# Performance work log

Hardware: AMD Instinct MI355X
Metric: run time of the kernel (lower is better)

## Reference

```python
import jax, jax.numpy as jnp
import numpy as np

B, L, D = 16, 2048, 320          # batch, frames, stacked feature dim (80 mel * 4 reduction)
CODEBOOK_SIZE, CODEBOOK_DIM = 8192, 16


def setup_inputs() -> dict:
    key = jax.random.key(0)
    k1, k2, k3 = jax.random.split(key, 3)
    masked_target_values = jax.random.normal(k1, (B, L, D), dtype=jnp.float32)
    # xavier_uniform_ for shape (D, codebook_dim): bound = sqrt(6/(fan_in+fan_out))
    bound = np.sqrt(6.0 / (D + CODEBOOK_DIM)).astype(np.float32)
    project_mat = jax.random.uniform(k2, (D, CODEBOOK_DIM), dtype=jnp.float32,
                                     minval=-bound, maxval=bound)
    cb = jax.random.normal(k3, (CODEBOOK_SIZE, CODEBOOK_DIM), dtype=jnp.float32)
    codebook_norm = cb / jnp.maximum(jnp.linalg.norm(cb, axis=-1, keepdims=True), 1e-12)
    return {"masked_target_values": masked_target_values,
            "project_mat": project_mat,
            "codebook_norm": codebook_norm}


def reference(masked_target_values, project_mat, codebook_norm):
    # project: (B, L, D) @ (D, K) -> (B, L, K)
    targets = jnp.einsum('bld,dk->blk', masked_target_values, project_mat)
    # L2 normalize along last dim (torch F.normalize with eps=1e-12)
    targets_norm = targets / jnp.maximum(
        jnp.linalg.norm(targets, axis=-1, keepdims=True), 1e-12)
    x2 = jnp.sum(targets_norm * targets_norm, axis=-1, keepdims=True)      # (B, L, 1)
    c2 = jnp.sum(codebook_norm * codebook_norm, axis=-1)                   # (C,)
    xc = jnp.einsum('blk,ck->blc', targets_norm, codebook_norm)            # (B, L, C)
    d2 = jnp.maximum(x2 + c2[None, None, :] - 2.0 * xc, 0.0)
    vector_distances = jnp.sqrt(d2)
    labels = jnp.argmin(vector_distances, axis=-1)                         # (B, L) int
    return labels
```

## Files before the change

kernel.cpp:

```cpp
#include <hip/hip_runtime.h>
#include <cfloat>

#define TOKENS 32768
#define DIM    320
#define NCODE  8192
#define PROW   20
#define APAD   40
#define NPAIRW 64
#define NWAVE  8
#define CERT_UNITS 34

typedef __attribute__((ext_vector_type(8)))  short short8;
typedef __attribute__((ext_vector_type(4)))  float f32x4;
typedef unsigned short ushort_t;
typedef unsigned int   uint_t;

static __device__ __forceinline__ ushort_t f2bf(float f) {
    uint_t u = __float_as_uint(f);
    u += 0x7fffu + ((u >> 16) & 1u);
    return (ushort_t)(u >> 16);
}
static __device__ __forceinline__ float bf2f(ushort_t h) {
    return __uint_as_float(((uint_t)h) << 16);
}
static __device__ __forceinline__ uint_t pack2(ushort_t a, ushort_t b) {
    return (uint_t)a | ((uint_t)b << 16);
}
static __device__ __forceinline__ int imaxi(int a, int b) { return a > b ? a : b; }
static __device__ __forceinline__ int imini(int a, int b) { return a < b ? a : b; }
static __device__ __forceinline__ int med3i(int a, int b, int c) {
    int d; asm("v_med3_i32 %0, %1, %2, %3" : "=v"(d) : "v"(a), "v"(b), "v"(c)); return d;
}
static __device__ __forceinline__ int max3i(int a, int b, int c) {
    int d; asm("v_max3_i32 %0, %1, %2, %3" : "=v"(d) : "v"(a), "v"(b), "v"(c)); return d;
}

__global__ __launch_bounds__(256) void pack_kernel(
    const float* __restrict__ cb,
    float* __restrict__ c2o,
    ushort_t* __restrict__ cbpack)
{
    int j = blockIdx.x * 256 + threadIdx.x;
    const float4* cr4 = (const float4*)(cb + (size_t)j * 16);
    float4 c0 = cr4[0], c1 = cr4[1], c2v = cr4[2], c3 = cr4[3];
    float c[16] = {c0.x, c0.y, c0.z, c0.w, c1.x, c1.y, c1.z, c1.w,
                   c2v.x, c2v.y, c2v.z, c2v.w, c3.x, c3.y, c3.z, c3.w};
    float s = 0.f;
    #pragma unroll
    for (int k = 0; k < 16; ++k) s = fmaf(c[k], c[k], s);
    c2o[j] = s;
    ushort_t hi[16], lo[16];
    #pragma unroll
    for (int k = 0; k < 16; ++k) {
        hi[k] = f2bf(c[k]);
        lo[k] = f2bf(c[k] - bf2f(hi[k]));
    }
    size_t base = (size_t)(j >> 4) * 512;
    int n = j & 15;
    *(uint4*)(cbpack + base + (size_t)(0 * 16 + n) * 8) =
        make_uint4(pack2(hi[0], hi[1]), pack2(hi[2], hi[3]),
                   pack2(hi[4], hi[5]), pack2(hi[6], hi[7]));
    *(uint4*)(cbpack + base + (size_t)(1 * 16 + n) * 8) =
        make_uint4(pack2(hi[8], hi[9]), pack2(hi[10], hi[11]),
                   pack2(hi[12], hi[13]), pack2(hi[14], hi[15]));
    *(uint4*)(cbpack + base + (size_t)(2 * 16 + n) * 8) =
        make_uint4(pack2(lo[0], lo[1]), pack2(lo[2], lo[3]),
                   pack2(lo[4], lo[5]), pack2(lo[6], lo[7]));
    *(uint4*)(cbpack + base + (size_t)(3 * 16 + n) * 8) =
        make_uint4(pack2(lo[8], lo[9]), pack2(lo[10], lo[11]),
                   pack2(lo[12], lo[13]), pack2(lo[14], lo[15]));
}

__global__ __launch_bounds__(512, 4) void fused_kernel(
    const float* __restrict__ x,
    const float* __restrict__ P,
    const float* __restrict__ cb,
    const float* __restrict__ c2g,
    const ushort_t* __restrict__ cbpack,
    int* __restrict__ out)
{
    __shared__ float Ps[DIM * PROW];
    __shared__ ushort_t ApackS[32 * APAD];
    __shared__ float tnS[32 * 16];
    __shared__ float x2S[32];
    __shared__ int mergeS[NWAVE][16][2];
    __shared__ int flagS[36];
    __shared__ float redE[NWAVE];
    __shared__ int   redI[NWAVE];

    int tid = threadIdx.x;
    int lane = tid & 63;
    int wave = tid >> 6;
    if (tid == 0) flagS[32] = 0;

    {
        const float4* P4 = (const float4*)P;
        #pragma unroll
        for (int i = 0; i < 3; ++i) {
            int idx = tid + i * 512;
            if (idx < 1280) {
                int row = idx >> 2, col = idx & 3;
                *(float4*)(Ps + row * PROW + col * 4) = P4[idx];
            }
        }
    }
    __syncthreads();

    int sub = tid & 15;
    int tk  = tid >> 4;
    int tok = blockIdx.x * 32 + tk;
    {
        const float* xr = x + (size_t)tok * DIM;
        float acc[16];
        #pragma unroll
        for (int k = 0; k < 16; ++k) acc[k] = 0.f;
        for (int i = 0; i < 20; ++i) {
            int d = i * 16 + sub;
            float xv = xr[d];
            const float4* pr = (const float4*)(Ps + d * PROW);
            float4 p0 = pr[0], p1 = pr[1], p2 = pr[2], p3 = pr[3];
            acc[0] = fmaf(xv, p0.x, acc[0]);   acc[1] = fmaf(xv, p0.y, acc[1]);
            acc[2] = fmaf(xv, p0.z, acc[2]);   acc[3] = fmaf(xv, p0.w, acc[3]);
            acc[4] = fmaf(xv, p1.x, acc[4]);   acc[5] = fmaf(xv, p1.y, acc[5]);
            acc[6] = fmaf(xv, p1.z, acc[6]);   acc[7] = fmaf(xv, p1.w, acc[7]);
            acc[8] = fmaf(xv, p2.x, acc[8]);   acc[9] = fmaf(xv, p2.y, acc[9]);
            acc[10] = fmaf(xv, p2.z, acc[10]); acc[11] = fmaf(xv, p2.w, acc[11]);
            acc[12] = fmaf(xv, p3.x, acc[12]); acc[13] = fmaf(xv, p3.y, acc[13]);
            acc[14] = fmaf(xv, p3.z, acc[14]); acc[15] = fmaf(xv, p3.w, acc[15]);
        }
        #pragma unroll
        for (int m = 1; m <= 8; m <<= 1) {
            #pragma unroll
            for (int k = 0; k < 16; ++k)
                acc[k] += __shfl_xor(acc[k], m);
        }
        float ss = 0.f;
        #pragma unroll
        for (int k = 0; k < 16; ++k) ss = fmaf(acc[k], acc[k], ss);
        float nrm = fmaxf(sqrtf(ss), 1e-12f);
        float inv = 1.0f / nrm;
        float t[16];
        #pragma unroll
        for (int k = 0; k < 16; ++k) t[k] = acc[k] * inv;
        float xx = 0.f;
        #pragma unroll
        for (int k = 0; k < 16; ++k) xx = fmaf(t[k], t[k], xx);

        ushort_t hi[16], lo[16];
        #pragma unroll
        for (int k = 0; k < 16; ++k) {
            float th = t[k] * 131072.0f;
            hi[k] = f2bf(th);
            lo[k] = f2bf(th - bf2f(hi[k]));
        }
        if (sub < 4) {
            *(float4*)(tnS + tk * 16 + sub * 4) =
                make_float4(t[4 * sub], t[4 * sub + 1], t[4 * sub + 2], t[4 * sub + 3]);
        }
        uint4* dst = (uint4*)(ApackS + tk * APAD);
        if (sub == 4) dst[0] = make_uint4(pack2(hi[0], hi[1]), pack2(hi[2], hi[3]),
                                          pack2(hi[4], hi[5]), pack2(hi[6], hi[7]));
        if (sub == 5) dst[1] = make_uint4(pack2(hi[8], hi[9]), pack2(hi[10], hi[11]),
                                          pack2(hi[12], hi[13]), pack2(hi[14], hi[15]));
        if (sub == 6) dst[2] = make_uint4(pack2(lo[0], lo[1]), pack2(lo[2], lo[3]),
                                          pack2(lo[4], lo[5]), pack2(lo[6], lo[7]));
        if (sub == 7) dst[3] = make_uint4(pack2(lo[8], lo[9]), pack2(lo[10], lo[11]),
                                          pack2(lo[12], lo[13]), pack2(lo[14], lo[15]));
        if (sub == 8) x2S[tk] = xx;
    }
    __syncthreads();

    int n    = lane & 15;
    int g    = lane >> 4;
    {
        int tokoff  = (wave >> 2) * 16;
        int wavebase = (wave & 3) * 2048;

        const ushort_t* ar = ApackS + (tokoff + n) * APAD;
        short8 a1 = *(const short8*)(ar + (g & 1) * 8);
        short8 a2 = *(const short8*)(ar + 16 + (g & 1) * 8);

        f32x4 zero = {};
        int p1[4], p2[4];
        #pragma unroll
        for (int r = 0; r < 4; ++r) { p1[r] = (int)0x80000000; p2[r] = (int)0x80000000; }

        const ushort_t* cpb = cbpack + (size_t)(wavebase >> 4) * 512 + (size_t)lane * 8;

#define LOADP(PIDX, BA, BB) do {                                           \
            const ushort_t* cp_ = cpb + (size_t)(PIDX) * 1024;             \
            (BA) = *(const short8*)(cp_);                                  \
            (BB) = *(const short8*)(cp_ + 512);                            \
        } while (0)

#define MFMAP(BA, BB, AA, AB) do {                                                    \
            (AA) = __builtin_amdgcn_mfma_f32_16x16x32_bf16(a1, (BA), zero, 0, 0, 0);  \
            (AA) = __builtin_amdgcn_mfma_f32_16x16x32_bf16(a2, (BA), (AA), 0, 0, 0);  \
            (AB) = __builtin_amdgcn_mfma_f32_16x16x32_bf16(a1, (BB), zero, 0, 0, 0);  \
            (AB) = __builtin_amdgcn_mfma_f32_16x16x32_bf16(a2, (BB), (AB), 0, 0, 0);  \
        } while (0)

#define EPIP(AA, AB, INV) do {                                             \
            _Pragma("unroll")                                              \
            for (int r = 0; r < 4; ++r) {                                  \
                int ka = (int)(AA)[r];                                     \
                int kb = (int)(AB)[r];                                     \
                int pa = (int)(((uint_t)ka << 13) | (uint_t)(INV));        \
                int pb = (int)(((uint_t)kb << 13) | (uint_t)((INV) - 16)); \
                int m3 = med3i(p1[r], pa, pb);                             \
                p1[r] = max3i(p1[r], pa, pb);                              \
                p2[r] = imaxi(p2[r], m3);                                  \
            }                                                              \
        } while (0)

        short8 Xa, Xb;
        short8 Ya, Yb;
        f32x4 aA0, aB0, aA1, aB1;

        LOADP(0, Xa, Xb);
        LOADP(1, Ya, Yb);
        MFMAP(Xa, Xb, aA0, aB0);
        int invA = 8191 - wavebase - n;

        #pragma unroll 1
        for (int k = 1; k < NPAIRW - 1; k += 2) {
            LOADP(k + 1, Xa, Xb);
            MFMAP(Ya, Yb, aA1, aB1);
            EPIP(aA0, aB0, invA);  invA -= 32;
            LOADP(k + 2, Ya, Yb);
            MFMAP(Xa, Xb, aA0, aB0);
            EPIP(aA1, aB1, invA);  invA -= 32;
        }
        MFMAP(Ya, Yb, aA1, aB1);
        EPIP(aA0, aB0, invA);  invA -= 32;
        EPIP(aA1, aB1, invA);

#undef LOADP
#undef MFMAP
#undef EPIP

        #pragma unroll
        for (int mask = 1; mask <= 8; mask <<= 1) {
            #pragma unroll
            for (int r = 0; r < 4; ++r) {
                int q1 = __shfl_xor(p1[r], mask);
                int q2 = __shfl_xor(p2[r], mask);
                int np2 = imaxi(imini(p1[r], q1), imaxi(p2[r], q2));
                p1[r] = imaxi(p1[r], q1);
                p2[r] = np2;
            }
        }
        #pragma unroll
        for (int r = 0; r < 4; ++r) {
            if (n == r) {
                mergeS[wave][g * 4 + r][0] = p1[r];
                mergeS[wave][g * 4 + r][1] = p2[r];
            }
        }
    }
    __syncthreads();

    if (tid < 32) {
        int wb = (tid >> 4) * 4;
        int i  = tid & 15;
        int p1 = mergeS[wb][i][0], p2 = mergeS[wb][i][1];
        #pragma unroll
        for (int w = 1; w < 4; ++w) {
            int q1 = mergeS[wb + w][i][0];
            int q2 = mergeS[wb + w][i][1];
            int np2 = imaxi(imini(p1, q1), imaxi(p2, q2));
            p1 = imaxi(p1, q1);
            p2 = np2;
        }
        if (((p1 >> 13) - (p2 >> 13)) <= CERT_UNITS) {
            int pz = atomicAdd(&flagS[32], 1);
            flagS[pz] = tid;
        } else {
            out[blockIdx.x * 32 + tid] = 8191 - (p1 & 8191);
        }
    }
    __syncthreads();

    int nf = flagS[32];
    for (int fi = 0; fi < nf; ++fi) {
        int ftk = flagS[fi];
        float a[16];
        #pragma unroll
        for (int k = 0; k < 16; ++k) a[k] = tnS[ftk * 16 + k];
        float xx = x2S[ftk];
        float mn = FLT_MAX;
        int   id = 0x7fffffff;
        for (int c = 0; c < 16; ++c) {
            int j = c * 512 + tid;
            const float4* c4 = (const float4*)(cb + (size_t)j * 16);
            float4 c0 = c4[0], c1 = c4[1], c2v = c4[2], c3 = c4[3];
            float dot = 0.f;
            dot = fmaf(a[0], c0.x, dot);   dot = fmaf(a[1], c0.y, dot);
            dot = fmaf(a[2], c0.z, dot);   dot = fmaf(a[3], c0.w, dot);
            dot = fmaf(a[4], c1.x, dot);   dot = fmaf(a[5], c1.y, dot);
            dot = fmaf(a[6], c1.z, dot);   dot = fmaf(a[7], c1.w, dot);
            dot = fmaf(a[8], c2v.x, dot);  dot = fmaf(a[9], c2v.y, dot);
            dot = fmaf(a[10], c2v.z, dot); dot = fmaf(a[11], c2v.w, dot);
            dot = fmaf(a[12], c3.x, dot);  dot = fmaf(a[13], c3.y, dot);
            dot = fmaf(a[14], c3.z, dot);  dot = fmaf(a[15], c3.w, dot);
            float e = fmaf(-2.f, dot, xx + c2g[j]);
            if (e < mn || (e == mn && j < id)) { mn = e; id = j; }
        }
        #pragma unroll
        for (int mask = 1; mask <= 32; mask <<= 1) {
            float pmn = __shfl_xor(mn, mask);
            int   pid = __shfl_xor(id, mask);
            if (pmn < mn || (pmn == mn && pid < id)) { mn = pmn; id = pid; }
        }
        if (lane == 0) { redE[wave] = mn; redI[wave] = id; }
        __syncthreads();
        if (tid == 0) {
            #pragma unroll
            for (int w = 1; w < NWAVE; ++w) {
                float pe = redE[w]; int pi = redI[w];
                if (pe < mn || (pe == mn && pi < id)) { mn = pe; id = pi; }
            }
            out[blockIdx.x * 32 + ftk] = id;
        }
        __syncthreads();
    }
}

extern "C" void kernel_launch(void* const* d_in, const int* in_sizes, int n_in,
                              void* d_out, int out_size, void* d_ws, size_t ws_size,
                              hipStream_t stream) {
    const float* x   = (const float*)d_in[0];
    const float* P   = (const float*)d_in[1];
    const float* cbn = (const float*)d_in[2];

    float*    c2     = (float*)d_ws;
    ushort_t* cbpack = (ushort_t*)(c2 + NCODE);
    int* labels = (int*)d_out;

    pack_kernel<<<NCODE / 256, 256, 0, stream>>>(cbn, c2, cbpack);
    fused_kernel<<<TOKENS / 32, 512, 0, stream>>>(x, P, cbn, c2, cbpack, labels);
}
```

Before: 162.4 us.

## Stage codebook chunks through LDS with async global_load_lds double buffering

New measurement: 172.7 us. +6.4%, slower.

```diff
diff --git a/kernel.cpp b/kernel.cpp
--- a/kernel.cpp
+++ b/kernel.cpp
@@ -6,7 +6,7 @@
 #define NCODE  8192
 #define PROW   20
 #define APAD   40
-#define NPAIRW 64
+#define NCHUNK 32
 #define NWAVE  8
 #define CERT_UNITS 34
 
@@ -14,6 +14,13 @@
 typedef __attribute__((ext_vector_type(4)))  float f32x4;
 typedef unsigned short ushort_t;
 typedef unsigned int   uint_t;
+
+typedef __attribute__((address_space(1))) const unsigned int gu32;
+typedef __attribute__((address_space(3))) unsigned int lu32;
+
+static __device__ __forceinline__ void stage1k(const ushort_t* g, ushort_t* l) {
+    __builtin_amdgcn_global_load_lds((gu32*)g, (lu32*)l, 16, 0, 0);
+}
 
 static __device__ __forceinline__ ushort_t f2bf(float f) {
     uint_t u = __float_as_uint(f);
@@ -79,7 +86,10 @@
     const ushort_t* __restrict__ cbpack,
     int* __restrict__ out)
 {
-    __shared__ float Ps[DIM * PROW];
+    __shared__ union {
+        float Ps[DIM * PROW];
+        ushort_t stage[2][8192];
+    } U;
     __shared__ ushort_t ApackS[32 * APAD];
     __shared__ float tnS[32 * 16];
     __shared__ float x2S[32];
@@ -100,7 +110,7 @@
             int idx = tid + i * 512;
             if (idx < 1280) {
                 int row = idx >> 2, col = idx & 3;
-                *(float4*)(Ps + row * PROW + col * 4) = P4[idx];
+                *(float4*)(U.Ps + row * PROW + col * 4) = P4[idx];
             }
         }
     }
@@ -117,7 +127,7 @@
         for (int i = 0; i < 20; ++i) {
             int d = i * 16 + sub;
             float xv = xr[d];
-            const float4* pr = (const float4*)(Ps + d * PROW);
+            const float4* pr = (const float4*)(U.Ps + d * PROW);
             float4 p0 = pr[0], p1 = pr[1], p2 = pr[2], p3 = pr[3];
             acc[0] = fmaf(xv, p0.x, acc[0]);   acc[1] = fmaf(xv, p0.y, acc[1]);
             acc[2] = fmaf(xv, p0.z, acc[2]);   acc[3] = fmaf(xv, p0.w, acc[3]);
@@ -170,11 +180,11 @@
     }
     __syncthreads();
 
-    int n    = lane & 15;
-    int g    = lane >> 4;
+    int n = lane & 15;
+    int g = lane >> 4;
     {
-        int tokoff  = (wave >> 2) * 16;
-        int wavebase = (wave & 3) * 2048;
+        int tokoff = (wave >> 2) * 16;
+        int q      = wave & 3;
 
         const ushort_t* ar = ApackS + (tokoff + n) * APAD;
         short8 a1 = *(const short8*)(ar + (g & 1) * 8);
@@ -185,59 +195,61 @@
         #pragma unroll
         for (int r = 0; r < 4; ++r) { p1[r] = (int)0x80000000; p2[r] = (int)0x80000000; }
 
-        const ushort_t* cpb = cbpack + (size_t)(wavebase >> 4) * 512 + (size_t)lane * 8;
-
-#define LOADP(PIDX, BA, BB) do {                                           \
-            const ushort_t* cp_ = cpb + (size_t)(PIDX) * 1024;             \
-            (BA) = *(const short8*)(cp_);                                  \
-            (BB) = *(const short8*)(cp_ + 512);                            \
-        } while (0)
-
-#define MFMAP(BA, BB, AA, AB) do {                                                    \
-            (AA) = __builtin_amdgcn_mfma_f32_16x16x32_bf16(a1, (BA), zero, 0, 0, 0);  \
-            (AA) = __builtin_amdgcn_mfma_f32_16x16x32_bf16(a2, (BA), (AA), 0, 0, 0);  \
-            (AB) = __builtin_amdgcn_mfma_f32_16x16x32_bf16(a1, (BB), zero, 0, 0, 0);  \
-            (AB) = __builtin_amdgcn_mfma_f32_16x16x32_bf16(a2, (BB), (AB), 0, 0, 0);  \
-        } while (0)
-
-#define EPIP(AA, AB, INV) do {                                             \
-            _Pragma("unroll")                                              \
-            for (int r = 0; r < 4; ++r) {                                  \
-                int ka = (int)(AA)[r];                                     \
-                int kb = (int)(AB)[r];                                     \
-                int pa = (int)(((uint_t)ka << 13) | (uint_t)(INV));        \
-                int pb = (int)(((uint_t)kb << 13) | (uint_t)((INV) - 16)); \
-                int m3 = med3i(p1[r], pa, pb);                             \
-                p1[r] = max3i(p1[r], pa, pb);                              \
-                p2[r] = imaxi(p2[r], m3);                                  \
-            }                                                              \
-        } while (0)
-
-        short8 Xa, Xb;
-        short8 Ya, Yb;
-        f32x4 aA0, aB0, aA1, aB1;
-
-        LOADP(0, Xa, Xb);
-        LOADP(1, Ya, Yb);
-        MFMAP(Xa, Xb, aA0, aB0);
-        int invA = 8191 - wavebase - n;
+        const ushort_t* gsrc = cbpack + (size_t)wave * 1024 + (size_t)lane * 8;
+
+        stage1k(gsrc,       &U.stage[0][wave * 1024]);
+        stage1k(gsrc + 512, &U.stage[0][wave * 1024 + 512]);
+        __syncthreads();
+
+        int cur = 0;
+        int invCh = 8191 - q * 64 - n;
 
         #pragma unroll 1
-        for (int k = 1; k < NPAIRW - 1; k += 2) {
-            LOADP(k + 1, Xa, Xb);
-            MFMAP(Ya, Yb, aA1, aB1);
-            EPIP(aA0, aB0, invA);  invA -= 32;
-            LOADP(k + 2, Ya, Yb);
-            MFMAP(Xa, Xb, aA0, aB0);
-            EPIP(aA1, aB1, invA);  invA -= 32;
-        }
-        MFMAP(Ya, Yb, aA1, aB1);
-        EPIP(aA0, aB0, invA);  invA -= 32;
-        EPIP(aA1, aB1, invA);
-
-#undef LOADP
-#undef MFMAP
-#undef EPIP
+        for (int ch = 0; ch < NCHUNK; ++ch) {
+            if (ch < NCHUNK - 1) {
+                const ushort_t* gs = gsrc + (size_t)(ch + 1) * 8192;
+                stage1k(gs,       &U.stage[cur ^ 1][wave * 1024]);
+                stage1k(gs + 512, &U.stage[cur ^ 1][wave * 1024 + 512]);
+            }
+            const ushort_t* sb = &U.stage[cur][q * 2048] + (size_t)lane * 8;
+            short8 b0 = *(const short8*)(sb);
+            short8 b1 = *(const short8*)(sb + 512);
+            short8 b2 = *(const short8*)(sb + 1024);
+            short8 b3 = *(const short8*)(sb + 1536);
+            f32x4 c0 = __builtin_amdgcn_mfma_f32_16x16x32_bf16(a1, b0, zero, 0, 0, 0);
+            c0 = __builtin_amdgcn_mfma_f32_16x16x32_bf16(a2, b0, c0, 0, 0, 0);
+            f32x4 c1 = __builtin_amdgcn_mfma_f32_16x16x32_bf16(a1, b1, zero, 0, 0, 0);
+            c1 = __builtin_amdgcn_mfma_f32_16x16x32_bf16(a2, b1, c1, 0, 0, 0);
+            f32x4 c2a = __builtin_amdgcn_mfma_f32_16x16x32_bf16(a1, b2, zero, 0, 0, 0);
+            c2a = __builtin_amdgcn_mfma_f32_16x16x32_bf16(a2, b2, c2a, 0, 0, 0);
+            f32x4 c3 = __builtin_amdgcn_mfma_f32_16x16x32_bf16(a1, b3, zero, 0, 0, 0);
+            c3 = __builtin_amdgcn_mfma_f32_16x16x32_bf16(a2, b3, c3, 0, 0, 0);
+
+            #pragma unroll
+            for (int r = 0; r < 4; ++r) {
+                int ka = (int)c0[r];
+                int kb = (int)c1[r];
+                int pa = (int)(((uint_t)ka << 13) | (uint_t)invCh);
+                int pb = (int)(((uint_t)kb << 13) | (uint_t)(invCh - 16));
+                int m3 = med3i(p1[r], pa, pb);
+                p1[r] = max3i(p1[r], pa, pb);
+                p2[r] = imaxi(p2[r], m3);
+            }
+            #pragma unroll
+            for (int r = 0; r < 4; ++r) {
+                int ka = (int)c2a[r];
+                int kb = (int)c3[r];
+                int pa = (int)(((uint_t)ka << 13) | (uint_t)(invCh - 32));
+                int pb = (int)(((uint_t)kb << 13) | (uint_t)(invCh - 48));
+                int m3 = med3i(p1[r], pa, pb);
+                p1[r] = max3i(p1[r], pa, pb);
+                p2[r] = imaxi(p2[r], m3);
+            }
+            invCh -= 256;
+
+            __syncthreads();
+            cur ^= 1;
+        }
 
         #pragma unroll
         for (int mask = 1; mask <= 8; mask <<= 1) {
```

## Split fused projection and codebook search into separate kernels

Applied to the files above, without the earlier changes.

After: 183.7 us. +13.2%, slower.

```diff
diff --git a/kernel.cpp b/kernel.cpp
--- a/kernel.cpp
+++ b/kernel.cpp
@@ -4,10 +4,7 @@
 #define TOKENS 32768
 #define DIM    320
 #define NCODE  8192
-#define PROW   20
-#define APAD   40
 #define NPAIRW 64
-#define NWAVE  8
 #define CERT_UNITS 34
 
 typedef __attribute__((ext_vector_type(8)))  short short8;
@@ -71,112 +68,101 @@
                    pack2(lo[12], lo[13]), pack2(lo[14], lo[15]));
 }
 
-__global__ __launch_bounds__(512, 4) void fused_kernel(
+__global__ __launch_bounds__(256) void project_kernel(
     const float* __restrict__ x,
     const float* __restrict__ P,
+    ushort_t* __restrict__ Apack,
+    float* __restrict__ tn,
+    float* __restrict__ x2)
+{
+    int tid = threadIdx.x;
+    int sub = tid & 15;
+    int tk  = tid >> 4;
+    int tok = blockIdx.x * 16 + tk;
+
+    const float* xr = x + (size_t)tok * DIM;
+    float acc[16];
+    #pragma unroll
+    for (int k = 0; k < 16; ++k) acc[k] = 0.f;
+    for (int i = 0; i < 20; ++i) {
+        int d = i * 16 + sub;
+        float xv = xr[d];
+        const float4* pr = (const float4*)(P + d * 16);
+        float4 p0 = pr[0], p1 = pr[1], p2 = pr[2], p3 = pr[3];
+        acc[0] = fmaf(xv, p0.x, acc[0]);   acc[1] = fmaf(xv, p0.y, acc[1]);
+        acc[2] = fmaf(xv, p0.z, acc[2]);   acc[3] = fmaf(xv, p0.w, acc[3]);
+        acc[4] = fmaf(xv, p1.x, acc[4]);   acc[5] = fmaf(xv, p1.y, acc[5]);
+        acc[6] = fmaf(xv, p1.z, acc[6]);   acc[7] = fmaf(xv, p1.w, acc[7]);
+        acc[8] = fmaf(xv, p2.x, acc[8]);   acc[9] = fmaf(xv, p2.y, acc[9]);
+        acc[10] = fmaf(xv, p2.z, acc[10]); acc[11] = fmaf(xv, p2.w, acc[11]);
+        acc[12] = fmaf(xv, p3.x, acc[12]); acc[13] = fmaf(xv, p3.y, acc[13]);
+        acc[14] = fmaf(xv, p3.z, acc[14]); acc[15] = fmaf(xv, p3.w, acc[15]);
+    }
+    #pragma unroll
+    for (int m = 1; m <= 8; m <<= 1) {
+        #pragma unroll
+        for (int k = 0; k < 16; ++k)
+            acc[k] += __shfl_xor(acc[k], m);
+    }
+    float ss = 0.f;
+    #pragma unroll
+    for (int k = 0; k < 16; ++k) ss = fmaf(acc[k], acc[k], ss);
+    float nrm = fmaxf(sqrtf(ss), 1e-12f);
+    float inv = 1.0f / nrm;
+    float t[16];
+    #pragma unroll
+    for (int k = 0; k < 16; ++k) t[k] = acc[k] * inv;
+    float xx = 0.f;
+    #pragma unroll
+    for (int k = 0; k < 16; ++k) xx = fmaf(t[k], t[k], xx);
+
+    ushort_t hi[16], lo[16];
+    #pragma unroll
+    for (int k = 0; k < 16; ++k) {
+        float th = t[k] * 131072.0f;
+        hi[k] = f2bf(th);
+        lo[k] = f2bf(th - bf2f(hi[k]));
+    }
+    if (sub < 4) {
+        *(float4*)(tn + (size_t)tok * 16 + sub * 4) =
+            make_float4(t[4 * sub], t[4 * sub + 1], t[4 * sub + 2], t[4 * sub + 3]);
+    }
+    uint4* dst = (uint4*)(Apack + (size_t)tok * 32);
+    if (sub == 4) dst[0] = make_uint4(pack2(hi[0], hi[1]), pack2(hi[2], hi[3]),
+                                      pack2(hi[4], hi[5]), pack2(hi[6], hi[7]));
+    if (sub == 5) dst[1] = make_uint4(pack2(hi[8], hi[9]), pack2(hi[10], hi[11]),
+                                      pack2(hi[12], hi[13]), pack2(hi[14], hi[15]));
+    if (sub == 6) dst[2] = make_uint4(pack2(lo[0], lo[1]), pack2(lo[2], lo[3]),
+                                      pack2(lo[4], lo[5]), pack2(lo[6], lo[7]));
+    if (sub == 7) dst[3] = make_uint4(pack2(lo[8], lo[9]), pack2(lo[10], lo[11]),
+                                      pack2(lo[12], lo[13]), pack2(lo[14], lo[15]));
+    if (sub == 8) x2[tok] = xx;
+}
+
+__global__ __launch_bounds__(256, 4) void search_kernel(
+    const ushort_t* __restrict__ Apack,
+    const ushort_t* __restrict__ cbpack,
     const float* __restrict__ cb,
     const float* __restrict__ c2g,
-    const ushort_t* __restrict__ cbpack,
+    const float* __restrict__ tn,
+    const float* __restrict__ x2g,
     int* __restrict__ out)
 {
-    __shared__ float Ps[DIM * PROW];
-    __shared__ ushort_t ApackS[32 * APAD];
-    __shared__ float tnS[32 * 16];
-    __shared__ float x2S[32];
-    __shared__ int mergeS[NWAVE][16][2];
-    __shared__ int flagS[36];
-    __shared__ float redE[NWAVE];
-    __shared__ int   redI[NWAVE];
-
-    int tid = threadIdx.x;
+    __shared__ int mergeS[4][16][2];
+    __shared__ int flagS[20];
+    __shared__ float redE[4];
+    __shared__ int   redI[4];
+
+    int tid  = threadIdx.x;
     int lane = tid & 63;
     int wave = tid >> 6;
-    if (tid == 0) flagS[32] = 0;
-
-    {
-        const float4* P4 = (const float4*)P;
-        #pragma unroll
-        for (int i = 0; i < 3; ++i) {
-            int idx = tid + i * 512;
-            if (idx < 1280) {
-                int row = idx >> 2, col = idx & 3;
-                *(float4*)(Ps + row * PROW + col * 4) = P4[idx];
-            }
-        }
-    }
-    __syncthreads();
-
-    int sub = tid & 15;
-    int tk  = tid >> 4;
-    int tok = blockIdx.x * 32 + tk;
-    {
-        const float* xr = x + (size_t)tok * DIM;
-        float acc[16];
-        #pragma unroll
-        for (int k = 0; k < 16; ++k) acc[k] = 0.f;
-        for (int i = 0; i < 20; ++i) {
-            int d = i * 16 + sub;
-            float xv = xr[d];
-            const float4* pr = (const float4*)(Ps + d * PROW);
-            float4 p0 = pr[0], p1 = pr[1], p2 = pr[2], p3 = pr[3];
-            acc[0] = fmaf(xv, p0.x, acc[0]);   acc[1] = fmaf(xv, p0.y, acc[1]);
-            acc[2] = fmaf(xv, p0.z, acc[2]);   acc[3] = fmaf(xv, p0.w, acc[3]);
-            acc[4] = fmaf(xv, p1.x, acc[4]);   acc[5] = fmaf(xv, p1.y, acc[5]);
-            acc[6] = fmaf(xv, p1.z, acc[6]);   acc[7] = fmaf(xv, p1.w, acc[7]);
-            acc[8] = fmaf(xv, p2.x, acc[8]);   acc[9] = fmaf(xv, p2.y, acc[9]);
-            acc[10] = fmaf(xv, p2.z, acc[10]); acc[11] = fmaf(xv, p2.w, acc[11]);
-            acc[12] = fmaf(xv, p3.x, acc[12]); acc[13] = fmaf(xv, p3.y, acc[13]);
-            acc[14] = fmaf(xv, p3.z, acc[14]); acc[15] = fmaf(xv, p3.w, acc[15]);
-        }
-        #pragma unroll
-        for (int m = 1; m <= 8; m <<= 1) {
-            #pragma unroll
-            for (int k = 0; k < 16; ++k)
-                acc[k] += __shfl_xor(acc[k], m);
-        }
-        float ss = 0.f;
-        #pragma unroll
-        for (int k = 0; k < 16; ++k) ss = fmaf(acc[k], acc[k], ss);
-        float nrm = fmaxf(sqrtf(ss), 1e-12f);
-        float inv = 1.0f / nrm;
-        float t[16];
-        #pragma unroll
-        for (int k = 0; k < 16; ++k) t[k] = acc[k] * inv;
-        float xx = 0.f;
-        #pragma unroll
-        for (int k = 0; k < 16; ++k) xx = fmaf(t[k], t[k], xx);
-
-        ushort_t hi[16], lo[16];
-        #pragma unroll
-        for (int k = 0; k < 16; ++k) {
-            float th = t[k] * 131072.0f;
-            hi[k] = f2bf(th);
-            lo[k] = f2bf(th - bf2f(hi[k]));
-        }
-        if (sub < 4) {
-            *(float4*)(tnS + tk * 16 + sub * 4) =
-                make_float4(t[4 * sub], t[4 * sub + 1], t[4 * sub + 2], t[4 * sub + 3]);
-        }
-        uint4* dst = (uint4*)(ApackS + tk * APAD);
-        if (sub == 4) dst[0] = make_uint4(pack2(hi[0], hi[1]), pack2(hi[2], hi[3]),
-                                          pack2(hi[4], hi[5]), pack2(hi[6], hi[7]));
-        if (sub == 5) dst[1] = make_uint4(pack2(hi[8], hi[9]), pack2(hi[10], hi[11]),
-                                          pack2(hi[12], hi[13]), pack2(hi[14], hi[15]));
-        if (sub == 6) dst[2] = make_uint4(pack2(lo[0], lo[1]), pack2(lo[2], lo[3]),
-                                          pack2(lo[4], lo[5]), pack2(lo[6], lo[7]));
-        if (sub == 7) dst[3] = make_uint4(pack2(lo[8], lo[9]), pack2(lo[10], lo[11]),
-                                          pack2(lo[12], lo[13]), pack2(lo[14], lo[15]));
-        if (sub == 8) x2S[tk] = xx;
-    }
-    __syncthreads();
-
     int n    = lane & 15;
     int g    = lane >> 4;
+    if (tid == 0) flagS[16] = 0;
+
+    int tokbase = blockIdx.x * 16;
     {
-        int tokoff  = (wave >> 2) * 16;
-        int wavebase = (wave & 3) * 2048;
-
-        const ushort_t* ar = ApackS + (tokoff + n) * APAD;
+        const ushort_t* ar = Apack + (size_t)(tokbase + n) * 32;
         short8 a1 = *(const short8*)(ar + (g & 1) * 8);
         short8 a2 = *(const short8*)(ar + 16 + (g & 1) * 8);
 
@@ -185,6 +171,7 @@
         #pragma unroll
         for (int r = 0; r < 4; ++r) { p1[r] = (int)0x80000000; p2[r] = (int)0x80000000; }
 
+        int wavebase = wave * 2048;
         const ushort_t* cpb = cbpack + (size_t)(wavebase >> 4) * 512 + (size_t)lane * 8;
 
 #define LOADP(PIDX, BA, BB) do {                                           \
@@ -260,38 +247,36 @@
     }
     __syncthreads();
 
-    if (tid < 32) {
-        int wb = (tid >> 4) * 4;
-        int i  = tid & 15;
-        int p1 = mergeS[wb][i][0], p2 = mergeS[wb][i][1];
+    if (tid < 16) {
+        int p1 = mergeS[0][tid][0], p2 = mergeS[0][tid][1];
         #pragma unroll
         for (int w = 1; w < 4; ++w) {
-            int q1 = mergeS[wb + w][i][0];
-            int q2 = mergeS[wb + w][i][1];
+            int q1 = mergeS[w][tid][0];
+            int q2 = mergeS[w][tid][1];
             int np2 = imaxi(imini(p1, q1), imaxi(p2, q2));
             p1 = imaxi(p1, q1);
             p2 = np2;
         }
         if (((p1 >> 13) - (p2 >> 13)) <= CERT_UNITS) {
-            int pz = atomicAdd(&flagS[32], 1);
+            int pz = atomicAdd(&flagS[16], 1);
             flagS[pz] = tid;
         } else {
-            out[blockIdx.x * 32 + tid] = 8191 - (p1 & 8191);
+            out[tokbase + tid] = 8191 - (p1 & 8191);
         }
     }
     __syncthreads();
 
-    int nf = flagS[32];
+    int nf = flagS[16];
     for (int fi = 0; fi < nf; ++fi) {
         int ftk = flagS[fi];
         float a[16];
         #pragma unroll
-        for (int k = 0; k < 16; ++k) a[k] = tnS[ftk * 16 + k];
-        float xx = x2S[ftk];
+        for (int k = 0; k < 16; ++k) a[k] = tn[(size_t)(tokbase + ftk) * 16 + k];
+        float xx = x2g[tokbase + ftk];
         float mn = FLT_MAX;
         int   id = 0x7fffffff;
-        for (int c = 0; c < 16; ++c) {
-            int j = c * 512 + tid;
+        for (int c = 0; c < 32; ++c) {
+            int j = c * 256 + tid;
             const float4* c4 = (const float4*)(cb + (size_t)j * 16);
             float4 c0 = c4[0], c1 = c4[1], c2v = c4[2], c3 = c4[3];
             float dot = 0.f;
@@ -316,11 +301,11 @@
         __syncthreads();
         if (tid == 0) {
             #pragma unroll
-            for (int w = 1; w < NWAVE; ++w) {
+            for (int w = 1; w < 4; ++w) {
                 float pe = redE[w]; int pi = redI[w];
                 if (pe < mn || (pe == mn && pi < id)) { mn = pe; id = pi; }
             }
-            out[blockIdx.x * 32 + ftk] = id;
+            out[tokbase + ftk] = id;
         }
         __syncthreads();
     }
@@ -335,8 +320,12 @@
 
     float*    c2     = (float*)d_ws;
     ushort_t* cbpack = (ushort_t*)(c2 + NCODE);
+    ushort_t* Apack  = cbpack + (size_t)NCODE * 32;
+    float*    tn     = (float*)(Apack + (size_t)TOKENS * 32);
+    float*    x2     = tn + (size_t)TOKENS * 16;
     int* labels = (int*)d_out;
 
     pack_kernel<<<NCODE / 256, 256, 0, stream>>>(cbn, c2, cbpack);
-    fused_kernel<<<TOKENS / 32, 512, 0, stream>>>(x, P, cbn, c2, cbpack, labels);
-}
+    project_kernel<<<TOKENS / 16, 256, 0, stream>>>(x, P, Apack, tn, x2);
+    search_kernel<<<TOKENS / 16, 256, 0, stream>>>(Apack, cbpack, cbn, c2, tn, x2, labels);
+}
```
